# Kernel optimization log

Hardware: AMD Instinct MI355X
Metric: run time of the kernel (lower is better)

Reference implementation:

```python
import jax, jax.numpy as jnp
import numpy as np

T, D, H, OUT = 32768, 1024, 2048, 1024
E, K = 8, 4
EPS = 1e-5


def setup_inputs() -> dict:
    key = jax.random.key(0)
    ks = jax.random.split(key, 10)
    s = 0.02
    return {
        "x": jax.random.normal(ks[0], (T, D), jnp.float32),
        "ln_gamma": jnp.ones((D,), jnp.float32),
        "ln_beta": jnp.zeros((D,), jnp.float32),
        "router_w": jax.random.normal(ks[1], (D, E), jnp.float32) * s,
        "router_b": jnp.zeros((E,), jnp.float32),
        "w1": jax.random.normal(ks[2], (E, D, H), jnp.float32) * s,
        "b1": jnp.zeros((E, H), jnp.float32),
        "w2": jax.random.normal(ks[3], (E, H, OUT), jnp.float32) * s,
        "b2": jnp.zeros((E, OUT), jnp.float32),
    }


def _layernorm(x, gamma, beta):
    mu = jnp.mean(x, axis=-1, keepdims=True)
    var = jnp.mean(jnp.square(x - mu), axis=-1, keepdims=True)
    return (x - mu) * jax.lax.rsqrt(var + EPS) * gamma + beta


def reference(x, ln_gamma, ln_beta, router_w, router_b, w1, b1, w2, b2):
    # pre-LayerNorm
    xn = _layernorm(x, ln_gamma, ln_beta)                      # [T, D]
    # router + top-k gate, softmax over the selected k logits
    logits = xn @ router_w + router_b                          # [T, E]
    top_vals, top_idx = jax.lax.top_k(logits, K)               # [T, K]
    gate = jax.nn.softmax(top_vals, axis=-1)                   # [T, K]
    # scatter gate weights back to dense [T, E] (top_idx unique per row)
    w_full = jnp.sum(jax.nn.one_hot(top_idx, E, dtype=gate.dtype) * gate[..., None], axis=-2)
    # streaming per-expert dense FFN + weighted accumulation (matches source)
    y = jnp.zeros((x.shape[0], OUT), dtype=x.dtype)
    for e in range(E):
        h = jax.nn.gelu(xn @ w1[e] + b1[e], approximate=False)  # [T, H]
        y = y + (h @ w2[e] + b2[e]) * w_full[:, e:e + 1]
    return y
```

## Files before the change

### kernel.cpp

```cpp
#include <hip/hip_runtime.h>
#include <hip/hip_bf16.h>
#include <math.h>

typedef unsigned short u16;
typedef __attribute__((ext_vector_type(8))) short short8;
typedef __attribute__((ext_vector_type(4))) float f32x4;
typedef __attribute__((ext_vector_type(4))) unsigned short u16x4;

constexpr int T_   = 32768;
constexpr int D_   = 1024;
constexpr int H_   = 2048;
constexpr int OUT_ = 1024;
constexpr int E_   = 8;
constexpr int MAXTILES_ = 1040;

__device__ __forceinline__ u16 f2bf(float f) {
    unsigned u = __float_as_uint(f);
    u += 0x7FFFu + ((u >> 16) & 1u);
    return (u16)(u >> 16);
}

__device__ __forceinline__ void gload_lds16(const u16* g, u16* l) {
    __builtin_amdgcn_global_load_lds(
        (const __attribute__((address_space(1))) unsigned int*)g,
        (__attribute__((address_space(3))) unsigned int*)l, 16, 0, 0);
}

__device__ __forceinline__ float gelu_exact(float v) {
    return 0.5f * v * (1.0f + erff(v * 0.70710678118654752f));
}

__global__ __launch_bounds__(256) void ln_router_kernel(
    const float* __restrict__ x, const float* __restrict__ gamma,
    const float* __restrict__ beta, const float* __restrict__ rw,
    const float* __restrict__ rb, u16* __restrict__ xn,
    unsigned* __restrict__ topk_idx, float* __restrict__ topk_gate)
{
    __shared__ float xn_lds[4 * 1024];
    __shared__ float rwT[8 * 1024];
    __shared__ float plog[4 * 32 * 8];

    const int tid  = threadIdx.x;
    const int lane = tid & 63;
    const int wave = tid >> 6;
    const int row  = blockIdx.x * 4 + wave;
    const float* xr = x + (size_t)row * D_;

#pragma unroll
    for (int it = 0; it < 8; ++it) {
        const int f0 = it * 1024 + tid * 4;
        float4 v4 = *(const float4*)(rw + f0);
        const int d  = f0 >> 3;
        const int e0 = (tid & 1) * 4;
        rwT[(e0 + 0) * 1024 + d] = v4.x;
        rwT[(e0 + 1) * 1024 + d] = v4.y;
        rwT[(e0 + 2) * 1024 + d] = v4.z;
        rwT[(e0 + 3) * 1024 + d] = v4.w;
    }

    float v[16];
#pragma unroll
    for (int j = 0; j < 4; ++j) {
        float4 t = *(const float4*)(xr + (j * 64 + lane) * 4);
        v[j*4+0] = t.x; v[j*4+1] = t.y; v[j*4+2] = t.z; v[j*4+3] = t.w;
    }
    float s = 0.f, ss = 0.f;
#pragma unroll
    for (int i = 0; i < 16; ++i) { s += v[i]; ss += v[i] * v[i]; }
#pragma unroll
    for (int st = 32; st > 0; st >>= 1) { s += __shfl_xor(s, st); ss += __shfl_xor(ss, st); }
    const float mu   = s * (1.0f / 1024.0f);
    const float var  = ss * (1.0f / 1024.0f) - mu * mu;
    const float rstd = rsqrtf(var + 1e-5f);

#pragma unroll
    for (int j = 0; j < 4; ++j) {
        const int d0 = (j * 64 + lane) * 4;
        float4 g4 = *(const float4*)(gamma + d0);
        float4 b4 = *(const float4*)(beta + d0);
        f32x4 xnv;
        xnv[0] = (v[j*4+0] - mu) * rstd * g4.x + b4.x;
        xnv[1] = (v[j*4+1] - mu) * rstd * g4.y + b4.y;
        xnv[2] = (v[j*4+2] - mu) * rstd * g4.z + b4.z;
        xnv[3] = (v[j*4+3] - mu) * rstd * g4.w + b4.w;
        *(f32x4*)(xn_lds + wave * 1024 + d0) = xnv;
        u16x4 pk;
        pk.x = f2bf(xnv[0]); pk.y = f2bf(xnv[1]);
        pk.z = f2bf(xnv[2]); pk.w = f2bf(xnv[3]);
        *(u16x4*)(xn + (size_t)row * D_ + d0) = pk;
    }
    __syncthreads();

    const int e    = lane >> 3;
    const int dseg = lane & 7;
    float part[4] = {0.f, 0.f, 0.f, 0.f};
#pragma unroll
    for (int ii = 0; ii < 8; ++ii) {
        const int q = dseg + (wave * 8 + ii) * 8;
        f32x4 rw4 = *(const f32x4*)(rwT + e * 1024 + q * 4);
#pragma unroll
        for (int r = 0; r < 4; ++r) {
            f32x4 x4 = *(const f32x4*)(xn_lds + r * 1024 + q * 4);
            part[r] += x4[0]*rw4[0] + x4[1]*rw4[1] + x4[2]*rw4[2] + x4[3]*rw4[3];
        }
    }
#pragma unroll
    for (int r = 0; r < 4; ++r)
        plog[(r * 32 + wave * 8 + dseg) * 8 + e] = part[r];
    __syncthreads();

    const int rr = wave;
    const int ee = (lane >> 3) & 7;
    const int s8 = lane & 7;
    float val = plog[(rr * 32 + s8) * 8 + ee] + plog[(rr * 32 + s8 + 8) * 8 + ee]
              + plog[(rr * 32 + s8 + 16) * 8 + ee] + plog[(rr * 32 + s8 + 24) * 8 + ee];
    val += __shfl_xor(val, 1);
    val += __shfl_xor(val, 2);
    val += __shfl_xor(val, 4);
    val += rb[ee];

    float vv[8];
#pragma unroll
    for (int k = 0; k < 8; ++k) vv[k] = __shfl(val, k * 8);

    if (lane == 0) {
        unsigned used = 0, pack = 0;
        float tv[4];
#pragma unroll
        for (int k = 0; k < 4; ++k) {
            float best = -3.4e38f; int bi = 0;
#pragma unroll
            for (int q = 0; q < 8; ++q)
                if (!((used >> q) & 1) && vv[q] > best) { best = vv[q]; bi = q; }
            used |= 1u << bi; tv[k] = best; pack |= (unsigned)bi << (8 * k);
        }
        float ex[4], sum = 0.f;
#pragma unroll
        for (int k = 0; k < 4; ++k) { ex[k] = expf(tv[k] - tv[0]); sum += ex[k]; }
        const float inv = 1.0f / sum;
        topk_idx[row] = pack;
#pragma unroll
        for (int k = 0; k < 4; ++k) topk_gate[row * 4 + k] = ex[k] * inv;
    }
}

__global__ __launch_bounds__(256) void transpose_cvt_kernel(
    const float* __restrict__ w1, const float* __restrict__ w2,
    u16* __restrict__ w1t, u16* __restrict__ w2t)
{
    __shared__ float lds[32][33];
    int t = blockIdx.x;
    const float* src; u16* dst; int R, C, rt, ct;
    if (t < 16384) {
        int e = t >> 11, loc = t & 2047;
        rt = loc >> 6; ct = loc & 63;
        src = w1 + (size_t)e * D_ * H_; dst = w1t + (size_t)e * D_ * H_;
        R = D_; C = H_;
    } else {
        t -= 16384;
        int e = t >> 11, loc = t & 2047;
        rt = loc >> 5; ct = loc & 31;
        src = w2 + (size_t)e * H_ * OUT_; dst = w2t + (size_t)e * H_ * OUT_;
        R = H_; C = OUT_;
    }
    const int r  = threadIdx.x >> 3;
    const int c4 = (threadIdx.x & 7) * 4;
    float4 val = *(const float4*)(src + (size_t)(rt * 32 + r) * C + ct * 32 + c4);
    lds[r][c4+0] = val.x; lds[r][c4+1] = val.y; lds[r][c4+2] = val.z; lds[r][c4+3] = val.w;
    __syncthreads();
    const int cc = threadIdx.x >> 3;
    const int r4 = (threadIdx.x & 7) * 4;
    u16x4 o;
    o.x = f2bf(lds[r4+0][cc]); o.y = f2bf(lds[r4+1][cc]);
    o.z = f2bf(lds[r4+2][cc]); o.w = f2bf(lds[r4+3][cc]);
    *(u16x4*)(dst + (size_t)(ct * 32 + cc) * R + rt * 32 + r4) = o;
}

__global__ __launch_bounds__(256) void pair_build_kernel(
    const unsigned* __restrict__ topk_idx, const float* __restrict__ topk_gate,
    int* __restrict__ pair_tok, float* __restrict__ pair_gate, int* __restrict__ gcount)
{
    __shared__ int lcnt[8], lbase[8];
    const int tok = blockIdx.x * 256 + threadIdx.x;
    if (threadIdx.x < 8) lcnt[threadIdx.x] = 0;
    __syncthreads();
    const unsigned pk = topk_idx[tok];
    int e[4], off[4]; float g[4];
#pragma unroll
    for (int k = 0; k < 4; ++k) {
        e[k] = (pk >> (8 * k)) & 255;
        g[k] = topk_gate[tok * 4 + k];
        off[k] = atomicAdd(&lcnt[e[k]], 1);
    }
    __syncthreads();
    if (threadIdx.x < 8) lbase[threadIdx.x] = atomicAdd(&gcount[threadIdx.x], lcnt[threadIdx.x]);
    __syncthreads();
#pragma unroll
    for (int k = 0; k < 4; ++k) {
        int pos = lbase[e[k]] + off[k];
        pair_tok[e[k] * T_ + pos]  = tok;
        pair_gate[e[k] * T_ + pos] = g[k];
    }
}

__global__ void scan_kernel(const int* __restrict__ gcount, int* __restrict__ meta)
{
    const int t = threadIdx.x;
    if (t < 8) {
        int tiles_before = 0, rows_before = 0;
        for (int i = 0; i < t; ++i) {
            int c = gcount[i];
            int nt = (c + 127) >> 7;
            tiles_before += nt; rows_before += nt << 7;
        }
        int c  = gcount[t];
        int nt = (c + 127) >> 7;
        meta[1 + t] = rows_before;
        for (int i = 0; i < nt; ++i) meta[32 + tiles_before + i] = (t << 16) | i;
        if (t == 7) meta[0] = tiles_before + nt;
    }
}

__global__ __launch_bounds__(256) void gemm1_grouped(
    const u16* __restrict__ xn, const u16* __restrict__ w1t,
    const float* __restrict__ b1, const int* __restrict__ pair_tok,
    const int* __restrict__ gcount, const int* __restrict__ meta,
    u16* __restrict__ h, int chunk_base)
{
    const int f    = blockIdx.x;
    const int tloc = (f >> 7) * 8 + (f & 7);
    const int nt   = (f >> 3) & 15;
    const int tile = chunk_base + tloc;
    if (tile >= meta[0]) return;
    const int dsc  = meta[32 + tile];
    const int e    = dsc >> 16;
    const int mloc = dsc & 0xffff;
    const int* ptok = pair_tok + e * T_;
    const u16* w1t_e = w1t + (size_t)e * D_ * H_;
    const float* b1_e = b1 + (size_t)e * H_;
    u16* hbase = h + (size_t)tloc * 128 * H_;

    __shared__ __align__(16) u16 As[128 * 32];
    __shared__ __align__(16) u16 Bs[128 * 32];

    const int tid  = threadIdx.x;
    const int lane = tid & 63;
    const int wave = tid >> 6;
    const int rs0 = tid >> 2;
    const int kg0 = (tid & 3) ^ ((rs0 >> 1) & 3);

    const int tokA0 = ptok[mloc * 128 + rs0];
    const int tokA1 = ptok[mloc * 128 + 64 + rs0];
    const u16* gA0 = xn + (size_t)tokA0 * D_ + kg0 * 8;
    const u16* gA1 = xn + (size_t)tokA1 * D_ + kg0 * 8;
    const u16* gB0 = w1t_e + (size_t)(nt * 128 + rs0) * D_ + kg0 * 8;
    const u16* gB1 = w1t_e + (size_t)(nt * 128 + 64 + rs0) * D_ + kg0 * 8;

    u16* AsW = As + wave * 512;
    u16* BsW = Bs + wave * 512;

    const int wm = (wave >> 1) * 64;
    const int wn = (wave & 1) * 64;
    const int fr = lane & 15;
    const int swz = (((lane >> 4) ^ ((fr >> 1) & 3))) * 8;

    f32x4 acc[4][4];
#pragma unroll
    for (int i = 0; i < 4; ++i)
#pragma unroll
        for (int j = 0; j < 4; ++j) acc[i][j] = (f32x4)0.0f;

    for (int kk = 0; kk < D_ / 32; ++kk) {
        gload_lds16(gA0, AsW);
        gload_lds16(gA1, AsW + 2048);
        gload_lds16(gB0, BsW);
        gload_lds16(gB1, BsW + 2048);
        gA0 += 32; gA1 += 32; gB0 += 32; gB1 += 32;
        __syncthreads();
        short8 a[4], b[4];
#pragma unroll
        for (int i = 0; i < 4; ++i) a[i] = *(const short8*)(As + (wm + i * 16 + fr) * 32 + swz);
#pragma unroll
        for (int i = 0; i < 4; ++i) b[i] = *(const short8*)(Bs + (wn + i * 16 + fr) * 32 + swz);
#pragma unroll
        for (int i = 0; i < 4; ++i)
#pragma unroll
            for (int j = 0; j < 4; ++j)
                acc[i][j] = __builtin_amdgcn_mfma_f32_16x16x32_bf16(a[i], b[j], acc[i][j], 0, 0, 0);
        __syncthreads();
    }

    const int cq = lane >> 4;
    const int cc = lane & 15;
#pragma unroll
    for (int j = 0; j < 4; ++j) {
        const int gcol = nt * 128 + wn + j * 16 + cc;
        const float bias = b1_e[gcol];
#pragma unroll
        for (int i = 0; i < 4; ++i) {
            const int lr0 = wm + i * 16 + cq * 4;
#pragma unroll
            for (int r = 0; r < 4; ++r) {
                float vv = gelu_exact(acc[i][j][r] + bias);
                hbase[(size_t)(lr0 + r) * H_ + gcol] = f2bf(vv);
            }
        }
    }
}

__global__ __launch_bounds__(256) void gemm2_grouped(
    const u16* __restrict__ h, const u16* __restrict__ w2t,
    const float* __restrict__ b2, const int* __restrict__ pair_tok,
    const float* __restrict__ pair_gate, const int* __restrict__ gcount,
    const int* __restrict__ meta, float* __restrict__ y, int chunk_base)
{
    const int f    = blockIdx.x;
    const int tloc = (f >> 6) * 8 + (f & 7);
    const int nt   = (f >> 3) & 7;
    const int tile = chunk_base + tloc;
    if (tile >= meta[0]) return;
    const int dsc  = meta[32 + tile];
    const int e    = dsc >> 16;
    const int mloc = dsc & 0xffff;
    const int count = gcount[e];
    const int* ptok = pair_tok + e * T_;
    const float* pgate = pair_gate + e * T_;
    const u16* w2t_e = w2t + (size_t)e * OUT_ * H_;
    const float* b2_e = b2 + (size_t)e * OUT_;
    const u16* hbase = h + (size_t)tloc * 128 * H_;

    __shared__ __align__(16) u16 As[128 * 32];
    __shared__ __align__(16) u16 Bs[128 * 32];

    const int tid  = threadIdx.x;
    const int lane = tid & 63;
    const int wave = tid >> 6;
    const int rs0 = tid >> 2;
    const int kg0 = (tid & 3) ^ ((rs0 >> 1) & 3);

    const u16* gA0 = hbase + (size_t)rs0 * H_ + kg0 * 8;
    const u16* gA1 = hbase + (size_t)(64 + rs0) * H_ + kg0 * 8;
    const u16* gB0 = w2t_e + (size_t)(nt * 128 + rs0) * H_ + kg0 * 8;
    const u16* gB1 = w2t_e + (size_t)(nt * 128 + 64 + rs0) * H_ + kg0 * 8;

    u16* AsW = As + wave * 512;
    u16* BsW = Bs + wave * 512;

    const int wm = (wave >> 1) * 64;
    const int wn = (wave & 1) * 64;
    const int fr = lane & 15;
    const int swz = (((lane >> 4) ^ ((fr >> 1) & 3))) * 8;

    f32x4 acc[4][4];
#pragma unroll
    for (int i = 0; i < 4; ++i)
#pragma unroll
        for (int j = 0; j < 4; ++j) acc[i][j] = (f32x4)0.0f;

    for (int kk = 0; kk < H_ / 32; ++kk) {
        gload_lds16(gA0, AsW);
        gload_lds16(gA1, AsW + 2048);
        gload_lds16(gB0, BsW);
        gload_lds16(gB1, BsW + 2048);
        gA0 += 32; gA1 += 32; gB0 += 32; gB1 += 32;
        __syncthreads();
        short8 a[4], b[4];
#pragma unroll
        for (int i = 0; i < 4; ++i) a[i] = *(const short8*)(As + (wm + i * 16 + fr) * 32 + swz);
#pragma unroll
        for (int i = 0; i < 4; ++i) b[i] = *(const short8*)(Bs + (wn + i * 16 + fr) * 32 + swz);
#pragma unroll
        for (int i = 0; i < 4; ++i)
#pragma unroll
            for (int j = 0; j < 4; ++j)
                acc[i][j] = __builtin_amdgcn_mfma_f32_16x16x32_bf16(a[i], b[j], acc[i][j], 0, 0, 0);
        __syncthreads();
    }

    const int cq = lane >> 4;
    const int cc = lane & 15;
    float b2v[4];
#pragma unroll
    for (int j = 0; j < 4; ++j) b2v[j] = b2_e[nt * 128 + wn + j * 16 + cc];
#pragma unroll
    for (int i = 0; i < 4; ++i) {
#pragma unroll
        for (int r = 0; r < 4; ++r) {
            const int lrow = wm + i * 16 + cq * 4 + r;
            if (mloc * 128 + lrow < count) {
                const int tok = ptok[mloc * 128 + lrow];
                const float g = pgate[mloc * 128 + lrow];
                float* yrow = y + (size_t)tok * OUT_;
#pragma unroll
                for (int j = 0; j < 4; ++j) {
                    const int gcol = nt * 128 + wn + j * 16 + cc;
                    atomicAdd(&yrow[gcol], g * (acc[i][j][r] + b2v[j]));
                }
            }
        }
    }
}

__global__ __launch_bounds__(256) void gemm1_kernel(
    const u16* __restrict__ xn, const u16* __restrict__ w1t_e,
    const float* __restrict__ b1_e, const int* __restrict__ ptok,
    const int* __restrict__ pcount, u16* __restrict__ h)
{
    const int count = *pcount;
    const int mt = blockIdx.y;
    if (mt * 128 >= count) return;
    const int nt = blockIdx.x;
    __shared__ __align__(16) u16 As[128 * 32];
    __shared__ __align__(16) u16 Bs[128 * 32];
    const int tid  = threadIdx.x;
    const int lane = tid & 63;
    const int wave = tid >> 6;
    const int rs0 = tid >> 2;
    const int kg0 = (tid & 3) ^ ((rs0 >> 1) & 3);
    const int tokA0 = ptok[mt * 128 + rs0];
    const int tokA1 = ptok[mt * 128 + 64 + rs0];
    const u16* gA0 = xn + (size_t)tokA0 * D_ + kg0 * 8;
    const u16* gA1 = xn + (size_t)tokA1 * D_ + kg0 * 8;
    const u16* gB0 = w1t_e + (size_t)(nt * 128 + rs0) * D_ + kg0 * 8;
    const u16* gB1 = w1t_e + (size_t)(nt * 128 + 64 + rs0) * D_ + kg0 * 8;
    u16* AsW = As + wave * 512;
    u16* BsW = Bs + wave * 512;
    const int wm = (wave >> 1) * 64;
    const int wn = (wave & 1) * 64;
    const int fr = lane & 15;
    const int swz = (((lane >> 4) ^ ((fr >> 1) & 3))) * 8;
    f32x4 acc[4][4];
#pragma unroll
    for (int i = 0; i < 4; ++i)
#pragma unroll
        for (int j = 0; j < 4; ++j) acc[i][j] = (f32x4)0.0f;
    for (int kk = 0; kk < D_ / 32; ++kk) {
        gload_lds16(gA0, AsW); gload_lds16(gA1, AsW + 2048);
        gload_lds16(gB0, BsW); gload_lds16(gB1, BsW + 2048);
        gA0 += 32; gA1 += 32; gB0 += 32; gB1 += 32;
        __syncthreads();
        short8 a[4], b[4];
#pragma unroll
        for (int i = 0; i < 4; ++i) a[i] = *(const short8*)(As + (wm + i * 16 + fr) * 32 + swz);
#pragma unroll
        for (int i = 0; i < 4; ++i) b[i] = *(const short8*)(Bs + (wn + i * 16 + fr) * 32 + swz);
#pragma unroll
        for (int i = 0; i < 4; ++i)
#pragma unroll
            for (int j = 0; j < 4; ++j)
                acc[i][j] = __builtin_amdgcn_mfma_f32_16x16x32_bf16(a[i], b[j], acc[i][j], 0, 0, 0);
        __syncthreads();
    }
    const int cq = lane >> 4;
    const int cc = lane & 15;
#pragma unroll
    for (int j = 0; j < 4; ++j) {
        const int gcol = nt * 128 + wn + j * 16 + cc;
        const float bias = b1_e[gcol];
#pragma unroll
        for (int i = 0; i < 4; ++i) {
            const int grow0 = mt * 128 + wm + i * 16 + cq * 4;
#pragma unroll
            for (int r = 0; r < 4; ++r) {
                float vv = gelu_exact(acc[i][j][r] + bias);
                h[(size_t)(grow0 + r) * H_ + gcol] = f2bf(vv);
            }
        }
    }
}

__global__ __launch_bounds__(256) void gemm2_kernel(
    const u16* __restrict__ h, const u16* __restrict__ w2t_e,
    const float* __restrict__ b2_e, const int* __restrict__ ptok,
    const float* __restrict__ pgate, const int* __restrict__ pcount,
    float* __restrict__ y)
{
    const int count = *pcount;
    const int mt = blockIdx.y;
    if (mt * 128 >= count) return;
    const int nt = blockIdx.x;
    __shared__ __align__(16) u16 As[128 * 32];
    __shared__ __align__(16) u16 Bs[128 * 32];
    const int tid  = threadIdx.x;
    const int lane = tid & 63;
    const int wave = tid >> 6;
    const int rs0 = tid >> 2;
    const int kg0 = (tid & 3) ^ ((rs0 >> 1) & 3);
    const u16* gA0 = h + (size_t)(mt * 128 + rs0) * H_ + kg0 * 8;
    const u16* gA1 = h + (size_t)(mt * 128 + 64 + rs0) * H_ + kg0 * 8;
    const u16* gB0 = w2t_e + (size_t)(nt * 128 + rs0) * H_ + kg0 * 8;
    const u16* gB1 = w2t_e + (size_t)(nt * 128 + 64 + rs0) * H_ + kg0 * 8;
    u16* AsW = As + wave * 512;
    u16* BsW = Bs + wave * 512;
    const int wm = (wave >> 1) * 64;
    const int wn = (wave & 1) * 64;
    const int fr = lane & 15;
    const int swz = (((lane >> 4) ^ ((fr >> 1) & 3))) * 8;
    f32x4 acc[4][4];
#pragma unroll
    for (int i = 0; i < 4; ++i)
#pragma unroll
        for (int j = 0; j < 4; ++j) acc[i][j] = (f32x4)0.0f;
    for (int kk = 0; kk < H_ / 32; ++kk) {
        gload_lds16(gA0, AsW); gload_lds16(gA1, AsW + 2048);
        gload_lds16(gB0, BsW); gload_lds16(gB1, BsW + 2048);
        gA0 += 32; gA1 += 32; gB0 += 32; gB1 += 32;
        __syncthreads();
        short8 a[4], b[4];
#pragma unroll
        for (int i = 0; i < 4; ++i) a[i] = *(const short8*)(As + (wm + i * 16 + fr) * 32 + swz);
#pragma unroll
        for (int i = 0; i < 4; ++i) b[i] = *(const short8*)(Bs + (wn + i * 16 + fr) * 32 + swz);
#pragma unroll
        for (int i = 0; i < 4; ++i)
#pragma unroll
            for (int j = 0; j < 4; ++j)
                acc[i][j] = __builtin_amdgcn_mfma_f32_16x16x32_bf16(a[i], b[j], acc[i][j], 0, 0, 0);
        __syncthreads();
    }
    const int cq = lane >> 4;
    const int cc = lane & 15;
#pragma unroll
    for (int i = 0; i < 4; ++i) {
#pragma unroll
        for (int r = 0; r < 4; ++r) {
            const int irow = mt * 128 + wm + i * 16 + cq * 4 + r;
            if (irow < count) {
                const int tok = ptok[irow];
                const float g = pgate[irow];
                float* yrow = y + (size_t)tok * OUT_;
#pragma unroll
                for (int j = 0; j < 4; ++j) {
                    const int gcol = nt * 128 + wn + j * 16 + cc;
                    yrow[gcol] += g * (acc[i][j][r] + b2_e[gcol]);
                }
            }
        }
    }
}

extern "C" void kernel_launch(void* const* d_in, const int* in_sizes, int n_in,
                              void* d_out, int out_size, void* d_ws, size_t ws_size,
                              hipStream_t stream)
{
    const float* x     = (const float*)d_in[0];
    const float* gamma = (const float*)d_in[1];
    const float* beta  = (const float*)d_in[2];
    const float* rw    = (const float*)d_in[3];
    const float* rb    = (const float*)d_in[4];
    const float* w1    = (const float*)d_in[5];
    const float* b1    = (const float*)d_in[6];
    const float* w2    = (const float*)d_in[7];
    const float* b2    = (const float*)d_in[8];
    float* y = (float*)d_out;

    char* ws = (char*)d_ws;
    const size_t xn_off   = 0;
    const size_t w1t_off  = 67108864;
    const size_t w2t_off  = 100663296;
    const size_t ptok_off = 134217728;
    const size_t pgat_off = 135266304;
    const size_t tidx_off = 136314880;
    const size_t tgat_off = 136445952;
    const size_t meta_off = 136970240;
    const size_t gcnt_off = 136978432;
    const size_t h_off    = 137363456;

    u16*      xn        = (u16*)(ws + xn_off);
    u16*      w1t       = (u16*)(ws + w1t_off);
    u16*      w2t       = (u16*)(ws + w2t_off);
    int*      pair_tok  = (int*)(ws + ptok_off);
    float*    pair_gate = (float*)(ws + pgat_off);
    unsigned* topk_idx  = (unsigned*)(ws + tidx_off);
    float*    topk_gate = (float*)(ws + tgat_off);
    int*      meta      = (int*)(ws + meta_off);
    int*      gcount    = (int*)(ws + gcnt_off);
    u16*      h         = (u16*)(ws + h_off);

    hipMemsetAsync(gcount, 0, 32, stream);
    hipMemsetAsync(pair_tok, 0, (size_t)E_ * T_ * 4, stream);
    hipMemsetAsync(d_out, 0, (size_t)T_ * OUT_ * 4, stream);

    ln_router_kernel<<<T_ / 4, 256, 0, stream>>>(x, gamma, beta, rw, rb, xn, topk_idx, topk_gate);
    transpose_cvt_kernel<<<32768, 256, 0, stream>>>(w1, w2, w1t, w2t);
    pair_build_kernel<<<T_ / 256, 256, 0, stream>>>(topk_idx, topk_gate, pair_tok, pair_gate, gcount);

    const size_t tile_bytes = (size_t)128 * H_ * 2;
    size_t avail = (ws_size > h_off) ? (ws_size - h_off) : 0;
    int CT = (int)(avail / tile_bytes);
    if (CT > 192) CT = 192;
    CT &= ~7;

    if (CT >= 64) {
        scan_kernel<<<1, 64, 0, stream>>>(gcount, meta);
        for (int base = 0; base < MAXTILES_; base += CT) {
            const int tiles = (MAXTILES_ - base < CT) ? (MAXTILES_ - base) : CT;
            gemm1_grouped<<<dim3(tiles * 16), 256, 0, stream>>>(
                xn, w1t, b1, pair_tok, gcount, meta, h, base);
            gemm2_grouped<<<dim3(tiles * 8), 256, 0, stream>>>(
                h, w2t, b2, pair_tok, pair_gate, gcount, meta, y, base);
        }
    } else {
        for (int e = 0; e < E_; ++e) {
            gemm1_kernel<<<dim3(H_ / 128, T_ / 128), 256, 0, stream>>>(
                xn, w1t + (size_t)e * H_ * D_, b1 + (size_t)e * H_,
                pair_tok + (size_t)e * T_, gcount + e, h);
            gemm2_kernel<<<dim3(OUT_ / 128, T_ / 128), 256, 0, stream>>>(
                h, w2t + (size_t)e * OUT_ * H_, b2 + (size_t)e * OUT_,
                pair_tok + (size_t)e * T_, pair_gate + (size_t)e * T_, gcount + e, y);
        }
    }
}
```

Baseline: 2.269 ms.

## Double-buffer LDS tiles in both expert GEMM kernels to overlap loads with MFMA

Both expert GEMM kernels get a second LDS buffer for the A and B tiles. The next K-slice is prefetched with global_load_lds while MFMAs run on the current slice, and one of the two barriers per iteration is removed. This is meant to hide global-load latency behind compute. In exchange LDS use doubles to 32KB per block, which may cut occupancy, and there is a correctness risk because the async LDS writes depend on the single remaining barrier for visibility.

```diff
diff --git a/kernel.cpp b/kernel.cpp
--- a/kernel.cpp
+++ b/kernel.cpp
@@ -240,8 +240,8 @@
     const float* b1_e = b1 + (size_t)e * H_;
     u16* hbase = h + (size_t)tloc * 128 * H_;
 
-    __shared__ __align__(16) u16 As[128 * 32];
-    __shared__ __align__(16) u16 Bs[128 * 32];
+    __shared__ __align__(16) u16 As[2 * 128 * 32];
+    __shared__ __align__(16) u16 Bs[2 * 128 * 32];
 
     const int tid  = threadIdx.x;
     const int lane = tid & 63;
@@ -270,24 +270,49 @@
 #pragma unroll
         for (int j = 0; j < 4; ++j) acc[i][j] = (f32x4)0.0f;
 
-    for (int kk = 0; kk < D_ / 32; ++kk) {
-        gload_lds16(gA0, AsW);
-        gload_lds16(gA1, AsW + 2048);
-        gload_lds16(gB0, BsW);
-        gload_lds16(gB1, BsW + 2048);
+    gload_lds16(gA0, AsW);
+    gload_lds16(gA1, AsW + 2048);
+    gload_lds16(gB0, BsW);
+    gload_lds16(gB1, BsW + 2048);
+    gA0 += 32; gA1 += 32; gB0 += 32; gB1 += 32;
+    __syncthreads();
+
+    int cur = 0;
+    for (int kk = 0; kk < D_ / 32 - 1; ++kk) {
+        const int nxt = cur ^ 1;
+        gload_lds16(gA0, AsW + nxt * 4096);
+        gload_lds16(gA1, AsW + nxt * 4096 + 2048);
+        gload_lds16(gB0, BsW + nxt * 4096);
+        gload_lds16(gB1, BsW + nxt * 4096 + 2048);
         gA0 += 32; gA1 += 32; gB0 += 32; gB1 += 32;
-        __syncthreads();
+        const u16* Ac = As + cur * 4096;
+        const u16* Bc = Bs + cur * 4096;
         short8 a[4], b[4];
 #pragma unroll
-        for (int i = 0; i < 4; ++i) a[i] = *(const short8*)(As + (wm + i * 16 + fr) * 32 + swz);
-#pragma unroll
-        for (int i = 0; i < 4; ++i) b[i] = *(const short8*)(Bs + (wn + i * 16 + fr) * 32 + swz);
+        for (int i = 0; i < 4; ++i) a[i] = *(const short8*)(Ac + (wm + i * 16 + fr) * 32 + swz);
+#pragma unroll
+        for (int i = 0; i < 4; ++i) b[i] = *(const short8*)(Bc + (wn + i * 16 + fr) * 32 + swz);
 #pragma unroll
         for (int i = 0; i < 4; ++i)
 #pragma unroll
             for (int j = 0; j < 4; ++j)
                 acc[i][j] = __builtin_amdgcn_mfma_f32_16x16x32_bf16(a[i], b[j], acc[i][j], 0, 0, 0);
         __syncthreads();
+        cur = nxt;
+    }
+    {
+        const u16* Ac = As + cur * 4096;
+        const u16* Bc = Bs + cur * 4096;
+        short8 a[4], b[4];
+#pragma unroll
+        for (int i = 0; i < 4; ++i) a[i] = *(const short8*)(Ac + (wm + i * 16 + fr) * 32 + swz);
+#pragma unroll
+        for (int i = 0; i < 4; ++i) b[i] = *(const short8*)(Bc + (wn + i * 16 + fr) * 32 + swz);
+#pragma unroll
+        for (int i = 0; i < 4; ++i)
+#pragma unroll
+            for (int j = 0; j < 4; ++j)
+                acc[i][j] = __builtin_amdgcn_mfma_f32_16x16x32_bf16(a[i], b[j], acc[i][j], 0, 0, 0);
     }
 
     const int cq = lane >> 4;
@@ -329,8 +354,8 @@
     const float* b2_e = b2 + (size_t)e * OUT_;
     const u16* hbase = h + (size_t)tloc * 128 * H_;
 
-    __shared__ __align__(16) u16 As[128 * 32];
-    __shared__ __align__(16) u16 Bs[128 * 32];
+    __shared__ __align__(16) u16 As[2 * 128 * 32];
+    __shared__ __align__(16) u16 Bs[2 * 128 * 32];
 
     const int tid  = threadIdx.x;
     const int lane = tid & 63;
@@ -357,24 +382,49 @@
 #pragma unroll
         for (int j = 0; j < 4; ++j) acc[i][j] = (f32x4)0.0f;
 
-    for (int kk = 0; kk < H_ / 32; ++kk) {
-        gload_lds16(gA0, AsW);
-        gload_lds16(gA1, AsW + 2048);
-        gload_lds16(gB0, BsW);
-        gload_lds16(gB1, BsW + 2048);
+    gload_lds16(gA0, AsW);
+    gload_lds16(gA1, AsW + 2048);
+    gload_lds16(gB0, BsW);
+    gload_lds16(gB1, BsW + 2048);
+    gA0 += 32; gA1 += 32; gB0 += 32; gB1 += 32;
+    __syncthreads();
+
+    int cur = 0;
+    for (int kk = 0; kk < H_ / 32 - 1; ++kk) {
+        const int nxt = cur ^ 1;
+        gload_lds16(gA0, AsW + nxt * 4096);
+        gload_lds16(gA1, AsW + nxt * 4096 + 2048);
+        gload_lds16(gB0, BsW + nxt * 4096);
+        gload_lds16(gB1, BsW + nxt * 4096 + 2048);
         gA0 += 32; gA1 += 32; gB0 += 32; gB1 += 32;
-        __syncthreads();
+        const u16* Ac = As + cur * 4096;
+        const u16* Bc = Bs + cur * 4096;
         short8 a[4], b[4];
 #pragma unroll
-        for (int i = 0; i < 4; ++i) a[i] = *(const short8*)(As + (wm + i * 16 + fr) * 32 + swz);
-#pragma unroll
-        for (int i = 0; i < 4; ++i) b[i] = *(const short8*)(Bs + (wn + i * 16 + fr) * 32 + swz);
+        for (int i = 0; i < 4; ++i) a[i] = *(const short8*)(Ac + (wm + i * 16 + fr) * 32 + swz);
+#pragma unroll
+        for (int i = 0; i < 4; ++i) b[i] = *(const short8*)(Bc + (wn + i * 16 + fr) * 32 + swz);
 #pragma unroll
         for (int i = 0; i < 4; ++i)
 #pragma unroll
             for (int j = 0; j < 4; ++j)
                 acc[i][j] = __builtin_amdgcn_mfma_f32_16x16x32_bf16(a[i], b[j], acc[i][j], 0, 0, 0);
         __syncthreads();
+        cur = nxt;
+    }
+    {
+        const u16* Ac = As + cur * 4096;
+        const u16* Bc = Bs + cur * 4096;
+        short8 a[4], b[4];
+#pragma unroll
+        for (int i = 0; i < 4; ++i) a[i] = *(const short8*)(Ac + (wm + i * 16 + fr) * 32 + swz);
+#pragma unroll
+        for (int i = 0; i < 4; ++i) b[i] = *(const short8*)(Bc + (wn + i * 16 + fr) * 32 + swz);
+#pragma unroll
+        for (int i = 0; i < 4; ++i)
+#pragma unroll
+            for (int j = 0; j < 4; ++j)
+                acc[i][j] = __builtin_amdgcn_mfma_f32_16x16x32_bf16(a[i], b[j], acc[i][j], 0, 0, 0);
     }
 
     const int cq = lane >> 4;
```

Result: slower. 2.437 ms (+7.4%).

## Triple-buffer LDS in grouped GEMMs and use a fast polynomial GELU

Applied to the files above, without the earlier changes.

Replaces the single-buffered load/sync/compute loop in the grouped GEMM1 and GEMM2 kernels with a three-stage LDS ring. Global-to-LDS loads for later K-steps are issued ahead, and a partial vmcnt wait plus one barrier per step overlaps memory latency with MFMA work. Exact erf-based GELU is replaced by the Abramowitz-Stegun polynomial approximation using a hardware reciprocal and a fast exp, which cuts epilogue ALU cost at a small accuracy cost. LDS use per block triples, which may lower occupancy. The ring also relies on a single barrier per stage to prevent overwriting a buffer still being read.

```diff
diff --git a/kernel.cpp b/kernel.cpp
--- a/kernel.cpp
+++ b/kernel.cpp
@@ -26,8 +26,53 @@
         (__attribute__((address_space(3))) unsigned int*)l, 16, 0, 0);
 }
 
-__device__ __forceinline__ float gelu_exact(float v) {
-    return 0.5f * v * (1.0f + erff(v * 0.70710678118654752f));
+__device__ __forceinline__ float gelu_fast(float v) {
+    float x = fabsf(v) * 0.70710678118654752f;
+    float t = __builtin_amdgcn_rcpf(fmaf(0.3275911f, x, 1.0f));
+    float p = fmaf(t, 1.061405429f, -1.453152027f);
+    p = fmaf(t, p, 1.421413741f);
+    p = fmaf(t, p, -0.284496736f);
+    p = fmaf(t, p, 0.254829592f);
+    p *= t;
+    float er = 1.0f - p * __expf(-x * x);
+    er = copysignf(er, v);
+    return 0.5f * v * (1.0f + er);
+}
+
+__device__ __forceinline__ void stage4(const u16*& gA0, const u16*& gA1,
+                                       const u16*& gB0, const u16*& gB1,
+                                       u16* AsW, u16* BsW)
+{
+    gload_lds16(gA0, AsW);
+    gload_lds16(gA1, AsW + 2048);
+    gload_lds16(gB0, BsW);
+    gload_lds16(gB1, BsW + 2048);
+    gA0 += 32; gA1 += 32; gB0 += 32; gB1 += 32;
+}
+
+__device__ __forceinline__ void mfma_step(const u16* Ac, const u16* Bc,
+                                          int wm, int wn, int fr, int swz,
+                                          f32x4 (&acc)[4][4])
+{
+    short8 a[4], b[4];
+#pragma unroll
+    for (int i = 0; i < 4; ++i) a[i] = *(const short8*)(Ac + (wm + i * 16 + fr) * 32 + swz);
+#pragma unroll
+    for (int i = 0; i < 4; ++i) b[i] = *(const short8*)(Bc + (wn + i * 16 + fr) * 32 + swz);
+#pragma unroll
+    for (int i = 0; i < 4; ++i)
+#pragma unroll
+        for (int j = 0; j < 4; ++j)
+            acc[i][j] = __builtin_amdgcn_mfma_f32_16x16x32_bf16(a[i], b[j], acc[i][j], 0, 0, 0);
+}
+
+__device__ __forceinline__ void waitb4() {
+    asm volatile("s_waitcnt vmcnt(4)" ::: "memory");
+    __builtin_amdgcn_s_barrier();
+}
+__device__ __forceinline__ void waitb0() {
+    asm volatile("s_waitcnt vmcnt(0)" ::: "memory");
+    __builtin_amdgcn_s_barrier();
 }
 
 __global__ __launch_bounds__(256) void ln_router_kernel(
@@ -240,8 +285,8 @@
     const float* b1_e = b1 + (size_t)e * H_;
     u16* hbase = h + (size_t)tloc * 128 * H_;
 
-    __shared__ __align__(16) u16 As[128 * 32];
-    __shared__ __align__(16) u16 Bs[128 * 32];
+    __shared__ __align__(16) u16 As[3 * 4096];
+    __shared__ __align__(16) u16 Bs[3 * 4096];
 
     const int tid  = threadIdx.x;
     const int lane = tid & 63;
@@ -270,39 +315,36 @@
 #pragma unroll
         for (int j = 0; j < 4; ++j) acc[i][j] = (f32x4)0.0f;
 
-    for (int kk = 0; kk < D_ / 32; ++kk) {
-        gload_lds16(gA0, AsW);
-        gload_lds16(gA1, AsW + 2048);
-        gload_lds16(gB0, BsW);
-        gload_lds16(gB1, BsW + 2048);
-        gA0 += 32; gA1 += 32; gB0 += 32; gB1 += 32;
-        __syncthreads();
-        short8 a[4], b[4];
-#pragma unroll
-        for (int i = 0; i < 4; ++i) a[i] = *(const short8*)(As + (wm + i * 16 + fr) * 32 + swz);
-#pragma unroll
-        for (int i = 0; i < 4; ++i) b[i] = *(const short8*)(Bs + (wn + i * 16 + fr) * 32 + swz);
-#pragma unroll
-        for (int i = 0; i < 4; ++i)
-#pragma unroll
-            for (int j = 0; j < 4; ++j)
-                acc[i][j] = __builtin_amdgcn_mfma_f32_16x16x32_bf16(a[i], b[j], acc[i][j], 0, 0, 0);
-        __syncthreads();
-    }
+    stage4(gA0, gA1, gB0, gB1, AsW,        BsW);
+    stage4(gA0, gA1, gB0, gB1, AsW + 4096, BsW + 4096);
+
+#pragma unroll 1
+    for (int it = 0; it < 10; ++it) {
+        waitb4(); stage4(gA0, gA1, gB0, gB1, AsW + 8192, BsW + 8192);
+        mfma_step(As,        Bs,        wm, wn, fr, swz, acc);
+        waitb4(); stage4(gA0, gA1, gB0, gB1, AsW,        BsW);
+        mfma_step(As + 4096, Bs + 4096, wm, wn, fr, swz, acc);
+        waitb4(); stage4(gA0, gA1, gB0, gB1, AsW + 4096, BsW + 4096);
+        mfma_step(As + 8192, Bs + 8192, wm, wn, fr, swz, acc);
+    }
+    waitb4(); mfma_step(As,        Bs,        wm, wn, fr, swz, acc);
+    waitb0(); mfma_step(As + 4096, Bs + 4096, wm, wn, fr, swz, acc);
 
     const int cq = lane >> 4;
     const int cc = lane & 15;
-#pragma unroll
-    for (int j = 0; j < 4; ++j) {
-        const int gcol = nt * 128 + wn + j * 16 + cc;
-        const float bias = b1_e[gcol];
-#pragma unroll
-        for (int i = 0; i < 4; ++i) {
-            const int lr0 = wm + i * 16 + cq * 4;
-#pragma unroll
-            for (int r = 0; r < 4; ++r) {
-                float vv = gelu_exact(acc[i][j][r] + bias);
-                hbase[(size_t)(lr0 + r) * H_ + gcol] = f2bf(vv);
+    float bias[4];
+#pragma unroll
+    for (int j = 0; j < 4; ++j) bias[j] = b1_e[nt * 128 + wn + j * 16 + cc];
+#pragma unroll
+    for (int i = 0; i < 4; ++i) {
+        const int lr0 = wm + i * 16 + cq * 4;
+#pragma unroll
+        for (int r = 0; r < 4; ++r) {
+            u16* hrow = hbase + (size_t)(lr0 + r) * H_ + nt * 128 + wn;
+#pragma unroll
+            for (int j = 0; j < 4; ++j) {
+                float vv = gelu_fast(acc[i][j][r] + bias[j]);
+                hrow[j * 16 + cc] = f2bf(vv);
             }
         }
     }
@@ -329,8 +371,8 @@
     const float* b2_e = b2 + (size_t)e * OUT_;
     const u16* hbase = h + (size_t)tloc * 128 * H_;
 
-    __shared__ __align__(16) u16 As[128 * 32];
-    __shared__ __align__(16) u16 Bs[128 * 32];
+    __shared__ __align__(16) u16 As[3 * 4096];
+    __shared__ __align__(16) u16 Bs[3 * 4096];
 
     const int tid  = threadIdx.x;
     const int lane = tid & 63;
@@ -357,25 +399,24 @@
 #pragma unroll
         for (int j = 0; j < 4; ++j) acc[i][j] = (f32x4)0.0f;
 
-    for (int kk = 0; kk < H_ / 32; ++kk) {
-        gload_lds16(gA0, AsW);
-        gload_lds16(gA1, AsW + 2048);
-        gload_lds16(gB0, BsW);
-        gload_lds16(gB1, BsW + 2048);
-        gA0 += 32; gA1 += 32; gB0 += 32; gB1 += 32;
-        __syncthreads();
-        short8 a[4], b[4];
-#pragma unroll
-        for (int i = 0; i < 4; ++i) a[i] = *(const short8*)(As + (wm + i * 16 + fr) * 32 + swz);
-#pragma unroll
-        for (int i = 0; i < 4; ++i) b[i] = *(const short8*)(Bs + (wn + i * 16 + fr) * 32 + swz);
-#pragma unroll
-        for (int i = 0; i < 4; ++i)
-#pragma unroll
-            for (int j = 0; j < 4; ++j)
-                acc[i][j] = __builtin_amdgcn_mfma_f32_16x16x32_bf16(a[i], b[j], acc[i][j], 0, 0, 0);
-        __syncthreads();
-    }
+    stage4(gA0, gA1, gB0, gB1, AsW,        BsW);
+    stage4(gA0, gA1, gB0, gB1, AsW + 4096, BsW + 4096);
+
+#pragma unroll 1
+    for (int it = 0; it < 20; ++it) {
+        waitb4(); stage4(gA0, gA1, gB0, gB1, AsW + 8192, BsW + 8192);
+        mfma_step(As,        Bs,        wm, wn, fr, swz, acc);
+        waitb4(); stage4(gA0, gA1, gB0, gB1, AsW,        BsW);
+        mfma_step(As + 4096, Bs + 4096, wm, wn, fr, swz, acc);
+        waitb4(); stage4(gA0, gA1, gB0, gB1, AsW + 4096, BsW + 4096);
+        mfma_step(As + 8192, Bs + 8192, wm, wn, fr, swz, acc);
+    }
+    waitb4(); stage4(gA0, gA1, gB0, gB1, AsW + 8192, BsW + 8192);
+    mfma_step(As,        Bs,        wm, wn, fr, swz, acc);
+    waitb4(); stage4(gA0, gA1, gB0, gB1, AsW,        BsW);
+    mfma_step(As + 4096, Bs + 4096, wm, wn, fr, swz, acc);
+    waitb4(); mfma_step(As + 8192, Bs + 8192, wm, wn, fr, swz, acc);
+    waitb0(); mfma_step(As,        Bs,        wm, wn, fr, swz, acc);
 
     const int cq = lane >> 4;
     const int cc = lane & 15;
@@ -439,16 +480,7 @@
         gload_lds16(gB0, BsW); gload_lds16(gB1, BsW + 2048);
         gA0 += 32; gA1 += 32; gB0 += 32; gB1 += 32;
         __syncthreads();
-        short8 a[4], b[4];
-#pragma unroll
-        for (int i = 0; i < 4; ++i) a[i] = *(const short8*)(As + (wm + i * 16 + fr) * 32 + swz);
-#pragma unroll
-        for (int i = 0; i < 4; ++i) b[i] = *(const short8*)(Bs + (wn + i * 16 + fr) * 32 + swz);
-#pragma unroll
-        for (int i = 0; i < 4; ++i)
-#pragma unroll
-            for (int j = 0; j < 4; ++j)
-                acc[i][j] = __builtin_amdgcn_mfma_f32_16x16x32_bf16(a[i], b[j], acc[i][j], 0, 0, 0);
+        mfma_step(As, Bs, wm, wn, fr, swz, acc);
         __syncthreads();
     }
     const int cq = lane >> 4;
@@ -462,7 +494,7 @@
             const int grow0 = mt * 128 + wm + i * 16 + cq * 4;
 #pragma unroll
             for (int r = 0; r < 4; ++r) {
-                float vv = gelu_exact(acc[i][j][r] + bias);
+                float vv = gelu_fast(acc[i][j][r] + bias);
                 h[(size_t)(grow0 + r) * H_ + gcol] = f2bf(vv);
             }
         }
@@ -506,16 +538,7 @@
         gload_lds16(gB0, BsW); gload_lds16(gB1, BsW + 2048);
         gA0 += 32; gA1 += 32; gB0 += 32; gB1 += 32;
         __syncthreads();
-        short8 a[4], b[4];
-#pragma unroll
-        for (int i = 0; i < 4; ++i) a[i] = *(const short8*)(As + (wm + i * 16 + fr) * 32 + swz);
-#pragma unroll
-        for (int i = 0; i < 4; ++i) b[i] = *(const short8*)(Bs + (wn + i * 16 + fr) * 32 + swz);
-#pragma unroll
-        for (int i = 0; i < 4; ++i)
-#pragma unroll
-            for (int j = 0; j < 4; ++j)
-                acc[i][j] = __builtin_amdgcn_mfma_f32_16x16x32_bf16(a[i], b[j], acc[i][j], 0, 0, 0);
+        mfma_step(As, Bs, wm, wn, fr, swz, acc);
         __syncthreads();
     }
     const int cq = lane >> 4;
```

New measurement: 2.437 ms. 7.4% more time.

## Double K-tile depth to 64 in grouped GEMMs and use polynomial GELU

Applied to the files above, without the earlier changes.

The grouped GEMM1/GEMM2 kernels now stage a 128x64 K-slice per iteration instead of 128x32, with a new swizzled global-to-LDS load pattern and a two-substep MFMA helper. This halves the number of barrier pairs per tile and issues more loads per sync. Exact erf-based GELU is replaced by an Abramowitz-Stegun polynomial approximation using the hardware reciprocal and fast exp, which cuts epilogue transcendental cost at a small accuracy cost. LDS usage per block doubles, which may reduce occupancy.

```diff
diff --git a/kernel.cpp b/kernel.cpp
--- a/kernel.cpp
+++ b/kernel.cpp
@@ -26,8 +26,63 @@
         (__attribute__((address_space(3))) unsigned int*)l, 16, 0, 0);
 }
 
-__device__ __forceinline__ float gelu_exact(float v) {
-    return 0.5f * v * (1.0f + erff(v * 0.70710678118654752f));
+__device__ __forceinline__ float gelu_fast(float v) {
+    float x = fabsf(v) * 0.70710678118654752f;
+    float t = __builtin_amdgcn_rcpf(fmaf(0.3275911f, x, 1.0f));
+    float p = fmaf(t, 1.061405429f, -1.453152027f);
+    p = fmaf(t, p, 1.421413741f);
+    p = fmaf(t, p, -0.284496736f);
+    p = fmaf(t, p, 0.254829592f);
+    p *= t;
+    float er = 1.0f - p * __expf(-x * x);
+    er = copysignf(er, v);
+    return 0.5f * v * (1.0f + er);
+}
+
+__device__ __forceinline__ void mfma_step64(const u16* Ac, const u16* Bc,
+                                            int wm, int wn, int fr, int swz,
+                                            f32x4 (&acc)[4][4])
+{
+    {
+        short8 a[4], b[4];
+#pragma unroll
+        for (int i = 0; i < 4; ++i) a[i] = *(const short8*)(Ac + (wm + i * 16 + fr) * 64 + swz);
+#pragma unroll
+        for (int j = 0; j < 4; ++j) b[j] = *(const short8*)(Bc + (wn + j * 16 + fr) * 64 + swz);
+#pragma unroll
+        for (int i = 0; i < 4; ++i)
+#pragma unroll
+            for (int j = 0; j < 4; ++j)
+                acc[i][j] = __builtin_amdgcn_mfma_f32_16x16x32_bf16(a[i], b[j], acc[i][j], 0, 0, 0);
+    }
+    {
+        short8 a[4], b[4];
+#pragma unroll
+        for (int i = 0; i < 4; ++i) a[i] = *(const short8*)(Ac + (wm + i * 16 + fr) * 64 + 32 + swz);
+#pragma unroll
+        for (int j = 0; j < 4; ++j) b[j] = *(const short8*)(Bc + (wn + j * 16 + fr) * 64 + 32 + swz);
+#pragma unroll
+        for (int i = 0; i < 4; ++i)
+#pragma unroll
+            for (int j = 0; j < 4; ++j)
+                acc[i][j] = __builtin_amdgcn_mfma_f32_16x16x32_bf16(a[i], b[j], acc[i][j], 0, 0, 0);
+    }
+}
+
+__device__ __forceinline__ void mfma_step(const u16* Ac, const u16* Bc,
+                                          int wm, int wn, int fr, int swz,
+                                          f32x4 (&acc)[4][4])
+{
+    short8 a[4], b[4];
+#pragma unroll
+    for (int i = 0; i < 4; ++i) a[i] = *(const short8*)(Ac + (wm + i * 16 + fr) * 32 + swz);
+#pragma unroll
+    for (int i = 0; i < 4; ++i) b[i] = *(const short8*)(Bc + (wn + i * 16 + fr) * 32 + swz);
+#pragma unroll
+    for (int i = 0; i < 4; ++i)
+#pragma unroll
+        for (int j = 0; j < 4; ++j)
+            acc[i][j] = __builtin_amdgcn_mfma_f32_16x16x32_bf16(a[i], b[j], acc[i][j], 0, 0, 0);
 }
 
 __global__ __launch_bounds__(256) void ln_router_kernel(
@@ -240,24 +295,25 @@
     const float* b1_e = b1 + (size_t)e * H_;
     u16* hbase = h + (size_t)tloc * 128 * H_;
 
-    __shared__ __align__(16) u16 As[128 * 32];
-    __shared__ __align__(16) u16 Bs[128 * 32];
+    __shared__ __align__(16) u16 As[128 * 64];
+    __shared__ __align__(16) u16 Bs[128 * 64];
 
     const int tid  = threadIdx.x;
     const int lane = tid & 63;
     const int wave = tid >> 6;
-    const int rs0 = tid >> 2;
-    const int kg0 = (tid & 3) ^ ((rs0 >> 1) & 3);
-
-    const int tokA0 = ptok[mloc * 128 + rs0];
-    const int tokA1 = ptok[mloc * 128 + 64 + rs0];
-    const u16* gA0 = xn + (size_t)tokA0 * D_ + kg0 * 8;
-    const u16* gA1 = xn + (size_t)tokA1 * D_ + kg0 * 8;
-    const u16* gB0 = w1t_e + (size_t)(nt * 128 + rs0) * D_ + kg0 * 8;
-    const u16* gB1 = w1t_e + (size_t)(nt * 128 + 64 + rs0) * D_ + kg0 * 8;
-
-    u16* AsW = As + wave * 512;
-    u16* BsW = Bs + wave * 512;
+
+    const int row32 = tid >> 3;
+    const int cslot = tid & 7;
+    const int key   = (row32 >> 1) & 3;
+    const int gc    = (cslot & 4) | ((cslot & 3) ^ key);
+
+    const u16* gA[4]; const u16* gB[4];
+#pragma unroll
+    for (int t = 0; t < 4; ++t) {
+        const int r = t * 32 + row32;
+        gA[t] = xn + (size_t)ptok[mloc * 128 + r] * D_ + gc * 8;
+        gB[t] = w1t_e + (size_t)(nt * 128 + r) * D_ + gc * 8;
+    }
 
     const int wm = (wave >> 1) * 64;
     const int wn = (wave & 1) * 64;
@@ -270,39 +326,33 @@
 #pragma unroll
         for (int j = 0; j < 4; ++j) acc[i][j] = (f32x4)0.0f;
 
-    for (int kk = 0; kk < D_ / 32; ++kk) {
-        gload_lds16(gA0, AsW);
-        gload_lds16(gA1, AsW + 2048);
-        gload_lds16(gB0, BsW);
-        gload_lds16(gB1, BsW + 2048);
-        gA0 += 32; gA1 += 32; gB0 += 32; gB1 += 32;
-        __syncthreads();
-        short8 a[4], b[4];
-#pragma unroll
-        for (int i = 0; i < 4; ++i) a[i] = *(const short8*)(As + (wm + i * 16 + fr) * 32 + swz);
-#pragma unroll
-        for (int i = 0; i < 4; ++i) b[i] = *(const short8*)(Bs + (wn + i * 16 + fr) * 32 + swz);
-#pragma unroll
-        for (int i = 0; i < 4; ++i)
-#pragma unroll
-            for (int j = 0; j < 4; ++j)
-                acc[i][j] = __builtin_amdgcn_mfma_f32_16x16x32_bf16(a[i], b[j], acc[i][j], 0, 0, 0);
+    for (int kk = 0; kk < D_ / 64; ++kk) {
+#pragma unroll
+        for (int t = 0; t < 4; ++t) {
+            gload_lds16(gA[t], As + t * 2048 + wave * 512);
+            gload_lds16(gB[t], Bs + t * 2048 + wave * 512);
+            gA[t] += 64; gB[t] += 64;
+        }
+        __syncthreads();
+        mfma_step64(As, Bs, wm, wn, fr, swz, acc);
         __syncthreads();
     }
 
     const int cq = lane >> 4;
     const int cc = lane & 15;
-#pragma unroll
-    for (int j = 0; j < 4; ++j) {
-        const int gcol = nt * 128 + wn + j * 16 + cc;
-        const float bias = b1_e[gcol];
-#pragma unroll
-        for (int i = 0; i < 4; ++i) {
-            const int lr0 = wm + i * 16 + cq * 4;
-#pragma unroll
-            for (int r = 0; r < 4; ++r) {
-                float vv = gelu_exact(acc[i][j][r] + bias);
-                hbase[(size_t)(lr0 + r) * H_ + gcol] = f2bf(vv);
+    float bias[4];
+#pragma unroll
+    for (int j = 0; j < 4; ++j) bias[j] = b1_e[nt * 128 + wn + j * 16 + cc];
+#pragma unroll
+    for (int i = 0; i < 4; ++i) {
+        const int lr0 = wm + i * 16 + cq * 4;
+#pragma unroll
+        for (int r = 0; r < 4; ++r) {
+            u16* hrow = hbase + (size_t)(lr0 + r) * H_ + nt * 128 + wn;
+#pragma unroll
+            for (int j = 0; j < 4; ++j) {
+                float vv = gelu_fast(acc[i][j][r] + bias[j]);
+                hrow[j * 16 + cc] = f2bf(vv);
             }
         }
     }
@@ -329,22 +379,25 @@
     const float* b2_e = b2 + (size_t)e * OUT_;
     const u16* hbase = h + (size_t)tloc * 128 * H_;
 
-    __shared__ __align__(16) u16 As[128 * 32];
-    __shared__ __align__(16) u16 Bs[128 * 32];
+    __shared__ __align__(16) u16 As[128 * 64];
+    __shared__ __align__(16) u16 Bs[128 * 64];
 
     const int tid  = threadIdx.x;
     const int lane = tid & 63;
     const int wave = tid >> 6;
-    const int rs0 = tid >> 2;
-    const int kg0 = (tid & 3) ^ ((rs0 >> 1) & 3);
-
-    const u16* gA0 = hbase + (size_t)rs0 * H_ + kg0 * 8;
-    const u16* gA1 = hbase + (size_t)(64 + rs0) * H_ + kg0 * 8;
-    const u16* gB0 = w2t_e + (size_t)(nt * 128 + rs0) * H_ + kg0 * 8;
-    const u16* gB1 = w2t_e + (size_t)(nt * 128 + 64 + rs0) * H_ + kg0 * 8;
-
-    u16* AsW = As + wave * 512;
-    u16* BsW = Bs + wave * 512;
+
+    const int row32 = tid >> 3;
+    const int cslot = tid & 7;
+    const int key   = (row32 >> 1) & 3;
+    const int gc    = (cslot & 4) | ((cslot & 3) ^ key);
+
+    const u16* gA[4]; const u16* gB[4];
+#pragma unroll
+    for (int t = 0; t < 4; ++t) {
+        const int r = t * 32 + row32;
+        gA[t] = hbase + (size_t)r * H_ + gc * 8;
+        gB[t] = w2t_e + (size_t)(nt * 128 + r) * H_ + gc * 8;
+    }
 
     const int wm = (wave >> 1) * 64;
     const int wn = (wave & 1) * 64;
@@ -357,23 +410,15 @@
 #pragma unroll
         for (int j = 0; j < 4; ++j) acc[i][j] = (f32x4)0.0f;
 
-    for (int kk = 0; kk < H_ / 32; ++kk) {
-        gload_lds16(gA0, AsW);
-        gload_lds16(gA1, AsW + 2048);
-        gload_lds16(gB0, BsW);
-        gload_lds16(gB1, BsW + 2048);
-        gA0 += 32; gA1 += 32; gB0 += 32; gB1 += 32;
-        __syncthreads();
-        short8 a[4], b[4];
-#pragma unroll
-        for (int i = 0; i < 4; ++i) a[i] = *(const short8*)(As + (wm + i * 16 + fr) * 32 + swz);
-#pragma unroll
-        for (int i = 0; i < 4; ++i) b[i] = *(const short8*)(Bs + (wn + i * 16 + fr) * 32 + swz);
-#pragma unroll
-        for (int i = 0; i < 4; ++i)
-#pragma unroll
-            for (int j = 0; j < 4; ++j)
-                acc[i][j] = __builtin_amdgcn_mfma_f32_16x16x32_bf16(a[i], b[j], acc[i][j], 0, 0, 0);
+    for (int kk = 0; kk < H_ / 64; ++kk) {
+#pragma unroll
+        for (int t = 0; t < 4; ++t) {
+            gload_lds16(gA[t], As + t * 2048 + wave * 512);
+            gload_lds16(gB[t], Bs + t * 2048 + wave * 512);
+            gA[t] += 64; gB[t] += 64;
+        }
+        __syncthreads();
+        mfma_step64(As, Bs, wm, wn, fr, swz, acc);
         __syncthreads();
     }
 
@@ -439,16 +484,7 @@
         gload_lds16(gB0, BsW); gload_lds16(gB1, BsW + 2048);
         gA0 += 32; gA1 += 32; gB0 += 32; gB1 += 32;
         __syncthreads();
-        short8 a[4], b[4];
-#pragma unroll
-        for (int i = 0; i < 4; ++i) a[i] = *(const short8*)(As + (wm + i * 16 + fr) * 32 + swz);
-#pragma unroll
-        for (int i = 0; i < 4; ++i) b[i] = *(const short8*)(Bs + (wn + i * 16 + fr) * 32 + swz);
-#pragma unroll
-        for (int i = 0; i < 4; ++i)
-#pragma unroll
-            for (int j = 0; j < 4; ++j)
-                acc[i][j] = __builtin_amdgcn_mfma_f32_16x16x32_bf16(a[i], b[j], acc[i][j], 0, 0, 0);
+        mfma_step(As, Bs, wm, wn, fr, swz, acc);
         __syncthreads();
     }
     const int cq = lane >> 4;
@@ -462,7 +498,7 @@
             const int grow0 = mt * 128 + wm + i * 16 + cq * 4;
 #pragma unroll
             for (int r = 0; r < 4; ++r) {
-                float vv = gelu_exact(acc[i][j][r] + bias);
+                float vv = gelu_fast(acc[i][j][r] + bias);
                 h[(size_t)(grow0 + r) * H_ + gcol] = f2bf(vv);
             }
         }
@@ -506,16 +542,7 @@
         gload_lds16(gB0, BsW); gload_lds16(gB1, BsW + 2048);
         gA0 += 32; gA1 += 32; gB0 += 32; gB1 += 32;
         __syncthreads();
-        short8 a[4], b[4];
-#pragma unroll
-        for (int i = 0; i < 4; ++i) a[i] = *(const short8*)(As + (wm + i * 16 + fr) * 32 + swz);
-#pragma unroll
-        for (int i = 0; i < 4; ++i) b[i] = *(const short8*)(Bs + (wn + i * 16 + fr) * 32 + swz);
-#pragma unroll
-        for (int i = 0; i < 4; ++i)
-#pragma unroll
-            for (int j = 0; j < 4; ++j)
-                acc[i][j] = __builtin_amdgcn_mfma_f32_16x16x32_bf16(a[i], b[j], acc[i][j], 0, 0, 0);
+        mfma_step(As, Bs, wm, wn, fr, swz, acc);
         __syncthreads();
     }
     const int cq = lane >> 4;
```

New measurement: 2.282 ms. Within noise of the previous version (+0.6%).
